# Kernel tuning notes

Measured on AMD Instinct MI355X. Metric: run time of the kernel, lower is better.

## Reference

```python
import jax, jax.numpy as jnp
import numpy as np

B, D, ADA, INTER, RANK = 16, 2048, 1024, 1024, 8

def setup_inputs() -> dict:
    key = jax.random.key(0)
    ks = jax.random.split(key, 7)
    s = lambda fan_in: 1.0 / np.sqrt(fan_in)
    return {
        "x": jax.random.normal(ks[0], (B, D), jnp.float32),
        "ada_emb": jax.random.normal(ks[1], (B, ADA), jnp.float32),
        "base": jax.random.normal(ks[2], (D, D), jnp.float32),  # nn.Parameter(torch.randn)
        "w1": jax.random.normal(ks[3], (ADA, INTER), jnp.float32) * s(ADA),
        "b1": jax.random.normal(ks[4], (INTER,), jnp.float32) * s(ADA),
        "w2": jax.random.normal(ks[5], (INTER, D * RANK * 2), jnp.float32) * s(INTER),
        "b2": jax.random.normal(ks[6], (D * RANK * 2,), jnp.float32) * s(INTER),
    }

def reference(x, ada_emb, base, w1, b1, w2, b2):
    Bn, Dn = x.shape
    # gen_weight: Linear -> GELU (exact, erf-based as torch nn.GELU) -> Linear
    h = jax.nn.gelu(ada_emb @ w1 + b1, approximate=False)
    xw = h @ w2 + b2                               # [B, D*rank*2]
    x_a, x_b = jnp.split(xw, 2, axis=-1)
    r = x_a.shape[-1] // Dn
    x_a = x_a.reshape(Bn, Dn, r)                   # [B, D, r]
    x_b = x_b.reshape(Bn, Dn, r)                   # [B, D, r]
    # per-sample low-rank delta + base: layer[b,d,k] = base[d,k] + sum_r x_a[b,d,r]*x_b[b,k,r]
    layer = base[None, :, :] + jnp.einsum('bdr,bkr->bdk', x_a, x_b)  # [B, D, D]
    out = jnp.einsum('bc,bco->bo', x, layer)       # batched matvec
    return x + out                                 # residual
```

## Files before the change

kernel.cpp:

```cpp
#include <hip/hip_runtime.h>
#include <math.h>

#define BN 16
#define DN 2048
#define ADA 1024
#define INTER 1024
#define NW2 32768
#define HALFN 16384

__global__ void k1a(const float* __restrict__ ada, const float* __restrict__ w1,
                    float* __restrict__ h_pre) {
    const int j  = blockIdx.x * 256 + threadIdx.x;
    const int k0 = blockIdx.y * 32;
    __shared__ float a_lds[BN][32];
    for (int idx = threadIdx.x; idx < BN * 32; idx += 256) {
        int m = idx >> 5, kk = idx & 31;
        a_lds[m][kk] = ada[m * ADA + k0 + kk];
    }
    __syncthreads();
    float acc[BN];
#pragma unroll
    for (int m = 0; m < BN; ++m) acc[m] = 0.f;
    for (int kk = 0; kk < 32; ++kk) {
        float w = w1[(k0 + kk) * INTER + j];
#pragma unroll
        for (int m = 0; m < BN; ++m) acc[m] += a_lds[m][kk] * w;
    }
#pragma unroll
    for (int m = 0; m < BN; ++m) atomicAdd(&h_pre[m * INTER + j], acc[m]);
}

__global__ void k1bt(const float* __restrict__ h_pre, const float* __restrict__ b1,
                     float* __restrict__ h_t) {
    int i = blockIdx.x * 256 + threadIdx.x;
    int m = i >> 10, j = i & (INTER - 1);
    float v = h_pre[i] + b1[j];
    float g = 0.5f * v * (1.f + erff(v * 0.70710678118654752f));
    h_t[j * BN + m] = g;
}

#define K2ACC(i, hv) do { acc[i].x = fmaf((hv), w.x, acc[i].x); \
                          acc[i].y = fmaf((hv), w.y, acc[i].y); } while (0)
__global__ __launch_bounds__(256) void k2m(const float* __restrict__ h_t,
                                           const float* __restrict__ w2,
                                           float* __restrict__ p2) {
    const int n2 = blockIdx.x * 256 + threadIdx.x;
    const int k0 = blockIdx.y * 128;
    __shared__ float hl[128 * BN];
    {
        const float4* src = (const float4*)(h_t + k0 * BN);
        float4* dst = (float4*)hl;
        dst[threadIdx.x]       = src[threadIdx.x];
        dst[threadIdx.x + 256] = src[threadIdx.x + 256];
    }
    __syncthreads();
    float2 acc[BN];
#pragma unroll
    for (int m = 0; m < BN; ++m) acc[m] = make_float2(0.f, 0.f);
    const float2* wp = (const float2*)w2 + (size_t)k0 * (NW2 / 2) + n2;
#pragma unroll 8
    for (int k = 0; k < 128; ++k) {
        const float2 w = wp[(size_t)k * (NW2 / 2)];
        const float4* hk = (const float4*)(hl + k * BN);
        const float4 h0 = hk[0], h1 = hk[1], h2 = hk[2], h3 = hk[3];
        K2ACC(0,  h0.x); K2ACC(1,  h0.y); K2ACC(2,  h0.z); K2ACC(3,  h0.w);
        K2ACC(4,  h1.x); K2ACC(5,  h1.y); K2ACC(6,  h1.z); K2ACC(7,  h1.w);
        K2ACC(8,  h2.x); K2ACC(9,  h2.y); K2ACC(10, h2.z); K2ACC(11, h2.w);
        K2ACC(12, h3.x); K2ACC(13, h3.y); K2ACC(14, h3.z); K2ACC(15, h3.w);
    }
    float2* op = (float2*)p2 + (size_t)blockIdx.y * (BN * NW2 / 2) + n2;
#pragma unroll
    for (int m = 0; m < BN; ++m) op[(size_t)m * (NW2 / 2)] = acc[m];
}

__global__ void k2r(const float* __restrict__ p2, const float* __restrict__ b2,
                    float* __restrict__ xw) {
    const int i  = blockIdx.x * 256 + threadIdx.x;
    const int n4 = i & (NW2 / 4 - 1);
    float4 s = ((const float4*)b2)[n4];
    const float4* p = (const float4*)p2 + i;
#pragma unroll
    for (int ks = 0; ks < 8; ++ks) {
        float4 v = p[(size_t)ks * (BN * NW2 / 4)];
        s.x += v.x; s.y += v.y; s.z += v.z; s.w += v.w;
    }
    ((float4*)xw)[i] = s;
}

__global__ void k3(const float* __restrict__ x, const float* __restrict__ xw,
                   float* __restrict__ t) {
    const int m = blockIdx.x >> 3, r = blockIdx.x & 7;
    float s = 0.f;
    for (int c = threadIdx.x; c < DN; c += 256)
        s += x[m * DN + c] * xw[(size_t)m * NW2 + c * 8 + r];
    __shared__ float red[256];
    red[threadIdx.x] = s;
    __syncthreads();
    for (int off = 128; off > 0; off >>= 1) {
        if (threadIdx.x < off) red[threadIdx.x] += red[threadIdx.x + off];
        __syncthreads();
    }
    if (threadIdx.x == 0) t[m * 8 + r] = red[0];
}

#define K4ACC(i, xv) do { acc[i].x = fmaf((xv), b.x, acc[i].x); \
                          acc[i].y = fmaf((xv), b.y, acc[i].y); \
                          acc[i].z = fmaf((xv), b.z, acc[i].z); \
                          acc[i].w = fmaf((xv), b.w, acc[i].w); } while (0)
__global__ __launch_bounds__(128) void k4m(const float* __restrict__ x,
                                           const float* __restrict__ base,
                                           float* __restrict__ p4) {
    const int o4 = blockIdx.x * 128 + threadIdx.x;
    const int c0 = blockIdx.y * 32;
    __shared__ float xt[32 * BN];
    for (int idx = threadIdx.x; idx < 32 * BN; idx += 128) {
        int cc = idx >> 4, m = idx & 15;
        xt[idx] = x[m * DN + c0 + cc];
    }
    __syncthreads();
    float4 acc[BN];
#pragma unroll
    for (int m = 0; m < BN; ++m) acc[m] = make_float4(0.f, 0.f, 0.f, 0.f);
    const float4* bp = (const float4*)base + (size_t)c0 * (DN / 4) + o4;
#pragma unroll 4
    for (int cc = 0; cc < 32; ++cc) {
        const float4 b = bp[(size_t)cc * (DN / 4)];
        const float4* xk = (const float4*)(xt + cc * BN);
        const float4 x0 = xk[0], x1 = xk[1], x2 = xk[2], x3 = xk[3];
        K4ACC(0,  x0.x); K4ACC(1,  x0.y); K4ACC(2,  x0.z); K4ACC(3,  x0.w);
        K4ACC(4,  x1.x); K4ACC(5,  x1.y); K4ACC(6,  x1.z); K4ACC(7,  x1.w);
        K4ACC(8,  x2.x); K4ACC(9,  x2.y); K4ACC(10, x2.z); K4ACC(11, x2.w);
        K4ACC(12, x3.x); K4ACC(13, x3.y); K4ACC(14, x3.z); K4ACC(15, x3.w);
    }
    float4* op = (float4*)p4 + (size_t)blockIdx.y * (BN * DN / 4) + o4;
#pragma unroll
    for (int m = 0; m < BN; ++m) op[m * (DN / 4)] = acc[m];
}

__global__ void k5(const float* __restrict__ x, const float* __restrict__ p4,
                   const float* __restrict__ xw, const float* __restrict__ t,
                   float* __restrict__ out) {
    const int i = blockIdx.x * 256 + threadIdx.x;
    const int m = i >> 11, o = i & (DN - 1);
    float s = x[i];
    const float* p = p4 + i;
#pragma unroll 8
    for (int ks = 0; ks < 64; ++ks) s += p[ks * (BN * DN)];
    const float4 xb0 = *(const float4*)(xw + (size_t)m * NW2 + HALFN + o * 8);
    const float4 xb1 = *(const float4*)(xw + (size_t)m * NW2 + HALFN + o * 8 + 4);
    const float* tm = t + m * 8;
    s += tm[0] * xb0.x + tm[1] * xb0.y + tm[2] * xb0.z + tm[3] * xb0.w
       + tm[4] * xb1.x + tm[5] * xb1.y + tm[6] * xb1.z + tm[7] * xb1.w;
    out[i] = s;
}

__global__ void k1b_o(const float* __restrict__ h_pre, const float* __restrict__ b1,
                      float* __restrict__ h) {
    int i = blockIdx.x * 256 + threadIdx.x;
    int j = i & (INTER - 1);
    float v = h_pre[i] + b1[j];
    h[i] = 0.5f * v * (1.f + erff(v * 0.70710678118654752f));
}

__global__ void k2_o(const float* __restrict__ h, const float* __restrict__ w2,
                     const float* __restrict__ b2, float* __restrict__ xw) {
    const int n  = blockIdx.x * 256 + threadIdx.x;
    const int k0 = blockIdx.y * 256;
    __shared__ float h_lds[BN][256];
    for (int idx = threadIdx.x; idx < BN * 256; idx += 256) {
        int m = idx >> 8, kk = idx & 255;
        h_lds[m][kk] = h[m * INTER + k0 + kk];
    }
    __syncthreads();
    const float init = (blockIdx.y == 0) ? b2[n] : 0.f;
    float acc[BN];
#pragma unroll
    for (int m = 0; m < BN; ++m) acc[m] = init;
    const float* w2p = w2 + (size_t)k0 * NW2 + n;
#pragma unroll 2
    for (int k4i = 0; k4i < 64; ++k4i) {
        float wa = w2p[(size_t)(4 * k4i + 0) * NW2];
        float wb = w2p[(size_t)(4 * k4i + 1) * NW2];
        float wc = w2p[(size_t)(4 * k4i + 2) * NW2];
        float wd = w2p[(size_t)(4 * k4i + 3) * NW2];
#pragma unroll
        for (int m = 0; m < BN; ++m) {
            const float4 hv = *reinterpret_cast<const float4*>(&h_lds[m][4 * k4i]);
            acc[m] += hv.x * wa + hv.y * wb + hv.z * wc + hv.w * wd;
        }
    }
#pragma unroll
    for (int m = 0; m < BN; ++m) atomicAdd(&xw[(size_t)m * NW2 + n], acc[m]);
}

__global__ void k4_o(const float* __restrict__ x, const float* __restrict__ base,
                     const float* __restrict__ xw, const float* __restrict__ t,
                     float* __restrict__ out) {
    const int o  = blockIdx.x * 256 + threadIdx.x;
    const int c0 = blockIdx.y * 64;
    __shared__ float x_lds[BN][64];
    for (int idx = threadIdx.x; idx < BN * 64; idx += 256) {
        int m = idx >> 6, cc = idx & 63;
        x_lds[m][cc] = x[m * DN + c0 + cc];
    }
    __syncthreads();
    float acc[BN];
#pragma unroll
    for (int m = 0; m < BN; ++m) acc[m] = 0.f;
    const float* bp = base + (size_t)c0 * DN + o;
#pragma unroll 2
    for (int c4 = 0; c4 < 16; ++c4) {
        float ba = bp[(size_t)(4 * c4 + 0) * DN];
        float bb = bp[(size_t)(4 * c4 + 1) * DN];
        float bc = bp[(size_t)(4 * c4 + 2) * DN];
        float bd = bp[(size_t)(4 * c4 + 3) * DN];
#pragma unroll
        for (int m = 0; m < BN; ++m) {
            const float4 xv = *reinterpret_cast<const float4*>(&x_lds[m][4 * c4]);
            acc[m] += xv.x * ba + xv.y * bb + xv.z * bc + xv.w * bd;
        }
    }
    if (blockIdx.y == 0) {
#pragma unroll
        for (int m = 0; m < BN; ++m) {
            const float4 xb0 = *reinterpret_cast<const float4*>(&xw[(size_t)m * NW2 + HALFN + o * 8]);
            const float4 xb1 = *reinterpret_cast<const float4*>(&xw[(size_t)m * NW2 + HALFN + o * 8 + 4]);
            float lr = t[m * 8 + 0] * xb0.x + t[m * 8 + 1] * xb0.y +
                       t[m * 8 + 2] * xb0.z + t[m * 8 + 3] * xb0.w +
                       t[m * 8 + 4] * xb1.x + t[m * 8 + 5] * xb1.y +
                       t[m * 8 + 6] * xb1.z + t[m * 8 + 7] * xb1.w;
            acc[m] += lr + x[m * DN + o];
        }
    }
#pragma unroll
    for (int m = 0; m < BN; ++m) atomicAdd(&out[m * DN + o], acc[m]);
}

extern "C" void kernel_launch(void* const* d_in, const int* in_sizes, int n_in,
                              void* d_out, int out_size, void* d_ws, size_t ws_size,
                              hipStream_t stream) {
    const float* x    = (const float*)d_in[0];
    const float* ada  = (const float*)d_in[1];
    const float* base = (const float*)d_in[2];
    const float* w1   = (const float*)d_in[3];
    const float* b1   = (const float*)d_in[4];
    const float* w2   = (const float*)d_in[5];
    const float* b2   = (const float*)d_in[6];
    float* out = (float*)d_out;
    char* ws = (char*)d_ws;

    const size_t NEED = 27394560;

    if (ws_size >= NEED) {
        float* p2    = (float*)(ws);
        float* xw    = (float*)(ws + 16777216);
        float* p4    = (float*)(ws + 18874368);
        float* h_pre = (float*)(ws + 27262976);
        float* h_t   = (float*)(ws + 27328512);
        float* t     = (float*)(ws + 27394048);

        hipMemsetAsync(h_pre, 0, 65536, stream);
        k1a <<<dim3(4, 32),  256, 0, stream>>>(ada, w1, h_pre);
        k1bt<<<64,           256, 0, stream>>>(h_pre, b1, h_t);
        k2m <<<dim3(64, 8),  256, 0, stream>>>(h_t, w2, p2);
        k4m <<<dim3(4, 64),  128, 0, stream>>>(x, base, p4);
        k2r <<<512,          256, 0, stream>>>(p2, b2, xw);
        k3  <<<128,          256, 0, stream>>>(x, xw, t);
        k5  <<<128,          256, 0, stream>>>(x, p4, xw, t, out);
    } else {
        float* xw    = (float*)(ws);
        float* h_pre = (float*)(ws + 2097152);
        float* h     = (float*)(ws + 2162688);
        float* t     = (float*)(ws + 2228224);
        hipMemsetAsync(ws, 0, 2162688, stream);
        hipMemsetAsync(d_out, 0, (size_t)out_size * sizeof(float), stream);
        k1a <<<dim3(4, 32),  256, 0, stream>>>(ada, w1, h_pre);
        k1b_o<<<64,          256, 0, stream>>>(h_pre, b1, h);
        k2_o<<<dim3(128, 4), 256, 0, stream>>>(h, w2, b2, xw);
        k3  <<<128,          256, 0, stream>>>(x, xw, t);
        k4_o<<<dim3(8, 32),  256, 0, stream>>>(x, base, xw, t, out);
    }
}
```

Baseline: 73.40 us.

## Register-prefetch weight streams in k2m/k4m, drop LDS staging, split batch in k4m

The w2 GEMV kernel and the base GEMV kernel now keep an 8-deep register ring of prefetched weight rows, so global loads are issued ahead of the FMAs that use them. Activations are read directly from global/cache rather than being staged in LDS behind a barrier. k4m moves to 256-thread blocks and splits the batch across blockIdx.z, cutting the accumulator count per thread to 8. The low-workspace fallback path is removed, so the code now assumes the large workspace is always available.

```diff
diff --git a/kernel.cpp b/kernel.cpp
--- a/kernel.cpp
+++ b/kernel.cpp
@@ -46,27 +46,33 @@
                                            float* __restrict__ p2) {
     const int n2 = blockIdx.x * 256 + threadIdx.x;
     const int k0 = blockIdx.y * 128;
-    __shared__ float hl[128 * BN];
-    {
-        const float4* src = (const float4*)(h_t + k0 * BN);
-        float4* dst = (float4*)hl;
-        dst[threadIdx.x]       = src[threadIdx.x];
-        dst[threadIdx.x + 256] = src[threadIdx.x + 256];
-    }
-    __syncthreads();
     float2 acc[BN];
 #pragma unroll
     for (int m = 0; m < BN; ++m) acc[m] = make_float2(0.f, 0.f);
+
     const float2* wp = (const float2*)w2 + (size_t)k0 * (NW2 / 2) + n2;
-#pragma unroll 8
-    for (int k = 0; k < 128; ++k) {
-        const float2 w = wp[(size_t)k * (NW2 / 2)];
-        const float4* hk = (const float4*)(hl + k * BN);
-        const float4 h0 = hk[0], h1 = hk[1], h2 = hk[2], h3 = hk[3];
-        K2ACC(0,  h0.x); K2ACC(1,  h0.y); K2ACC(2,  h0.z); K2ACC(3,  h0.w);
-        K2ACC(4,  h1.x); K2ACC(5,  h1.y); K2ACC(6,  h1.z); K2ACC(7,  h1.w);
-        K2ACC(8,  h2.x); K2ACC(9,  h2.y); K2ACC(10, h2.z); K2ACC(11, h2.w);
-        K2ACC(12, h3.x); K2ACC(13, h3.y); K2ACC(14, h3.z); K2ACC(15, h3.w);
+    const float4* hp = (const float4*)h_t + (size_t)k0 * 4;
+
+    float2 wbuf[8];
+#pragma unroll
+    for (int u = 0; u < 8; ++u) wbuf[u] = wp[(size_t)u * (NW2 / 2)];
+
+    for (int kb = 0; kb < 128; kb += 8) {
+#pragma unroll
+        for (int u = 0; u < 8; ++u) {
+            const int k = kb + u;
+            const float2 w = wbuf[u];
+            const int kn = (k + 8 < 128) ? (k + 8) : k;
+            wbuf[u] = wp[(size_t)kn * (NW2 / 2)];
+            const float4 h0 = hp[k * 4 + 0];
+            const float4 h1 = hp[k * 4 + 1];
+            const float4 h2 = hp[k * 4 + 2];
+            const float4 h3 = hp[k * 4 + 3];
+            K2ACC(0,  h0.x); K2ACC(1,  h0.y); K2ACC(2,  h0.z); K2ACC(3,  h0.w);
+            K2ACC(4,  h1.x); K2ACC(5,  h1.y); K2ACC(6,  h1.z); K2ACC(7,  h1.w);
+            K2ACC(8,  h2.x); K2ACC(9,  h2.y); K2ACC(10, h2.z); K2ACC(11, h2.w);
+            K2ACC(12, h3.x); K2ACC(13, h3.y); K2ACC(14, h3.z); K2ACC(15, h3.w);
+        }
     }
     float2* op = (float2*)p2 + (size_t)blockIdx.y * (BN * NW2 / 2) + n2;
 #pragma unroll
@@ -107,34 +113,44 @@
                           acc[i].y = fmaf((xv), b.y, acc[i].y); \
                           acc[i].z = fmaf((xv), b.z, acc[i].z); \
                           acc[i].w = fmaf((xv), b.w, acc[i].w); } while (0)
-__global__ __launch_bounds__(128) void k4m(const float* __restrict__ x,
+__global__ __launch_bounds__(256) void k4m(const float* __restrict__ x,
                                            const float* __restrict__ base,
                                            float* __restrict__ p4) {
-    const int o4 = blockIdx.x * 128 + threadIdx.x;
+    const int o4 = blockIdx.x * 256 + threadIdx.x;
     const int c0 = blockIdx.y * 32;
-    __shared__ float xt[32 * BN];
-    for (int idx = threadIdx.x; idx < 32 * BN; idx += 128) {
-        int cc = idx >> 4, m = idx & 15;
-        xt[idx] = x[m * DN + c0 + cc];
-    }
-    __syncthreads();
-    float4 acc[BN];
-#pragma unroll
-    for (int m = 0; m < BN; ++m) acc[m] = make_float4(0.f, 0.f, 0.f, 0.f);
+    const int m0 = blockIdx.z * 8;
+    float4 acc[8];
+#pragma unroll
+    for (int m = 0; m < 8; ++m) acc[m] = make_float4(0.f, 0.f, 0.f, 0.f);
+
     const float4* bp = (const float4*)base + (size_t)c0 * (DN / 4) + o4;
-#pragma unroll 4
-    for (int cc = 0; cc < 32; ++cc) {
-        const float4 b = bp[(size_t)cc * (DN / 4)];
-        const float4* xk = (const float4*)(xt + cc * BN);
-        const float4 x0 = xk[0], x1 = xk[1], x2 = xk[2], x3 = xk[3];
-        K4ACC(0,  x0.x); K4ACC(1,  x0.y); K4ACC(2,  x0.z); K4ACC(3,  x0.w);
-        K4ACC(4,  x1.x); K4ACC(5,  x1.y); K4ACC(6,  x1.z); K4ACC(7,  x1.w);
-        K4ACC(8,  x2.x); K4ACC(9,  x2.y); K4ACC(10, x2.z); K4ACC(11, x2.w);
-        K4ACC(12, x3.x); K4ACC(13, x3.y); K4ACC(14, x3.z); K4ACC(15, x3.w);
-    }
-    float4* op = (float4*)p4 + (size_t)blockIdx.y * (BN * DN / 4) + o4;
-#pragma unroll
-    for (int m = 0; m < BN; ++m) op[m * (DN / 4)] = acc[m];
+    float4 bbuf[8];
+#pragma unroll
+    for (int u = 0; u < 8; ++u) bbuf[u] = bp[(size_t)u * (DN / 4)];
+
+    for (int cb = 0; cb < 32; cb += 8) {
+#pragma unroll
+        for (int u = 0; u < 8; ++u) {
+            const int cc = cb + u;
+            const float4 b = bbuf[u];
+            const int cn = (cc + 8 < 32) ? (cc + 8) : cc;
+            bbuf[u] = bp[(size_t)cn * (DN / 4)];
+            const float x0 = x[(m0 + 0) * DN + c0 + cc];
+            const float x1 = x[(m0 + 1) * DN + c0 + cc];
+            const float x2 = x[(m0 + 2) * DN + c0 + cc];
+            const float x3 = x[(m0 + 3) * DN + c0 + cc];
+            const float x4 = x[(m0 + 4) * DN + c0 + cc];
+            const float x5 = x[(m0 + 5) * DN + c0 + cc];
+            const float x6 = x[(m0 + 6) * DN + c0 + cc];
+            const float x7 = x[(m0 + 7) * DN + c0 + cc];
+            K4ACC(0, x0); K4ACC(1, x1); K4ACC(2, x2); K4ACC(3, x3);
+            K4ACC(4, x4); K4ACC(5, x5); K4ACC(6, x6); K4ACC(7, x7);
+        }
+    }
+    float4* op = (float4*)p4 + (size_t)blockIdx.y * (BN * DN / 4)
+               + (size_t)m0 * (DN / 4) + o4;
+#pragma unroll
+    for (int m = 0; m < 8; ++m) op[(size_t)m * (DN / 4)] = acc[m];
 }
 
 __global__ void k5(const float* __restrict__ x, const float* __restrict__ p4,
@@ -154,88 +170,6 @@
     out[i] = s;
 }
 
-__global__ void k1b_o(const float* __restrict__ h_pre, const float* __restrict__ b1,
-                      float* __restrict__ h) {
-    int i = blockIdx.x * 256 + threadIdx.x;
-    int j = i & (INTER - 1);
-    float v = h_pre[i] + b1[j];
-    h[i] = 0.5f * v * (1.f + erff(v * 0.70710678118654752f));
-}
-
-__global__ void k2_o(const float* __restrict__ h, const float* __restrict__ w2,
-                     const float* __restrict__ b2, float* __restrict__ xw) {
-    const int n  = blockIdx.x * 256 + threadIdx.x;
-    const int k0 = blockIdx.y * 256;
-    __shared__ float h_lds[BN][256];
-    for (int idx = threadIdx.x; idx < BN * 256; idx += 256) {
-        int m = idx >> 8, kk = idx & 255;
-        h_lds[m][kk] = h[m * INTER + k0 + kk];
-    }
-    __syncthreads();
-    const float init = (blockIdx.y == 0) ? b2[n] : 0.f;
-    float acc[BN];
-#pragma unroll
-    for (int m = 0; m < BN; ++m) acc[m] = init;
-    const float* w2p = w2 + (size_t)k0 * NW2 + n;
-#pragma unroll 2
-    for (int k4i = 0; k4i < 64; ++k4i) {
-        float wa = w2p[(size_t)(4 * k4i + 0) * NW2];
-        float wb = w2p[(size_t)(4 * k4i + 1) * NW2];
-        float wc = w2p[(size_t)(4 * k4i + 2) * NW2];
-        float wd = w2p[(size_t)(4 * k4i + 3) * NW2];
-#pragma unroll
-        for (int m = 0; m < BN; ++m) {
-            const float4 hv = *reinterpret_cast<const float4*>(&h_lds[m][4 * k4i]);
-            acc[m] += hv.x * wa + hv.y * wb + hv.z * wc + hv.w * wd;
-        }
-    }
-#pragma unroll
-    for (int m = 0; m < BN; ++m) atomicAdd(&xw[(size_t)m * NW2 + n], acc[m]);
-}
-
-__global__ void k4_o(const float* __restrict__ x, const float* __restrict__ base,
-                     const float* __restrict__ xw, const float* __restrict__ t,
-                     float* __restrict__ out) {
-    const int o  = blockIdx.x * 256 + threadIdx.x;
-    const int c0 = blockIdx.y * 64;
-    __shared__ float x_lds[BN][64];
-    for (int idx = threadIdx.x; idx < BN * 64; idx += 256) {
-        int m = idx >> 6, cc = idx & 63;
-        x_lds[m][cc] = x[m * DN + c0 + cc];
-    }
-    __syncthreads();
-    float acc[BN];
-#pragma unroll
-    for (int m = 0; m < BN; ++m) acc[m] = 0.f;
-    const float* bp = base + (size_t)c0 * DN + o;
-#pragma unroll 2
-    for (int c4 = 0; c4 < 16; ++c4) {
-        float ba = bp[(size_t)(4 * c4 + 0) * DN];
-        float bb = bp[(size_t)(4 * c4 + 1) * DN];
-        float bc = bp[(size_t)(4 * c4 + 2) * DN];
-        float bd = bp[(size_t)(4 * c4 + 3) * DN];
-#pragma unroll
-        for (int m = 0; m < BN; ++m) {
-            const float4 xv = *reinterpret_cast<const float4*>(&x_lds[m][4 * c4]);
-            acc[m] += xv.x * ba + xv.y * bb + xv.z * bc + xv.w * bd;
-        }
-    }
-    if (blockIdx.y == 0) {
-#pragma unroll
-        for (int m = 0; m < BN; ++m) {
-            const float4 xb0 = *reinterpret_cast<const float4*>(&xw[(size_t)m * NW2 + HALFN + o * 8]);
-            const float4 xb1 = *reinterpret_cast<const float4*>(&xw[(size_t)m * NW2 + HALFN + o * 8 + 4]);
-            float lr = t[m * 8 + 0] * xb0.x + t[m * 8 + 1] * xb0.y +
-                       t[m * 8 + 2] * xb0.z + t[m * 8 + 3] * xb0.w +
-                       t[m * 8 + 4] * xb1.x + t[m * 8 + 5] * xb1.y +
-                       t[m * 8 + 6] * xb1.z + t[m * 8 + 7] * xb1.w;
-            acc[m] += lr + x[m * DN + o];
-        }
-    }
-#pragma unroll
-    for (int m = 0; m < BN; ++m) atomicAdd(&out[m * DN + o], acc[m]);
-}
-
 extern "C" void kernel_launch(void* const* d_in, const int* in_sizes, int n_in,
                               void* d_out, int out_size, void* d_ws, size_t ws_size,
                               hipStream_t stream) {
@@ -249,35 +183,20 @@
     float* out = (float*)d_out;
     char* ws = (char*)d_ws;
 
-    const size_t NEED = 27394560;
-
-    if (ws_size >= NEED) {
-        float* p2    = (float*)(ws);
-        float* xw    = (float*)(ws + 16777216);
-        float* p4    = (float*)(ws + 18874368);
-        float* h_pre = (float*)(ws + 27262976);
-        float* h_t   = (float*)(ws + 27328512);
-        float* t     = (float*)(ws + 27394048);
-
-        hipMemsetAsync(h_pre, 0, 65536, stream);
-        k1a <<<dim3(4, 32),  256, 0, stream>>>(ada, w1, h_pre);
-        k1bt<<<64,           256, 0, stream>>>(h_pre, b1, h_t);
-        k2m <<<dim3(64, 8),  256, 0, stream>>>(h_t, w2, p2);
-        k4m <<<dim3(4, 64),  128, 0, stream>>>(x, base, p4);
-        k2r <<<512,          256, 0, stream>>>(p2, b2, xw);
-        k3  <<<128,          256, 0, stream>>>(x, xw, t);
-        k5  <<<128,          256, 0, stream>>>(x, p4, xw, t, out);
-    } else {
-        float* xw    = (float*)(ws);
-        float* h_pre = (float*)(ws + 2097152);
-        float* h     = (float*)(ws + 2162688);
-        float* t     = (float*)(ws + 2228224);
-        hipMemsetAsync(ws, 0, 2162688, stream);
-        hipMemsetAsync(d_out, 0, (size_t)out_size * sizeof(float), stream);
-        k1a <<<dim3(4, 32),  256, 0, stream>>>(ada, w1, h_pre);
-        k1b_o<<<64,          256, 0, stream>>>(h_pre, b1, h);
-        k2_o<<<dim3(128, 4), 256, 0, stream>>>(h, w2, b2, xw);
-        k3  <<<128,          256, 0, stream>>>(x, xw, t);
-        k4_o<<<dim3(8, 32),  256, 0, stream>>>(x, base, xw, t, out);
-    }
-}
+    float* p2    = (float*)(ws);
+    float* xw    = (float*)(ws + 16777216);
+    float* p4    = (float*)(ws + 18874368);
+    float* h_pre = (float*)(ws + 27262976);
+    float* h_t   = (float*)(ws + 27328512);
+    float* t     = (float*)(ws + 27394048);
+
+    hipMemsetAsync(h_pre, 0, 65536, stream);
+
+    k1a <<<dim3(4, 32),    256, 0, stream>>>(ada, w1, h_pre);
+    k1bt<<<64,             256, 0, stream>>>(h_pre, b1, h_t);
+    k2m <<<dim3(64, 8),    256, 0, stream>>>(h_t, w2, p2);
+    k4m <<<dim3(2, 64, 2), 256, 0, stream>>>(x, base, p4);
+    k2r <<<512,            256, 0, stream>>>(p2, b2, xw);
+    k3  <<<128,            256, 0, stream>>>(x, xw, t);
+    k5  <<<128,            256, 0, stream>>>(x, p4, xw, t, out);
+}
```

New measurement: 71.05 us. 1.03x faster.
